# Kernel tuning notes

Hardware: AMD Instinct MI355X
Metric: run time of the kernel (lower is better)

Reference implementation:

```python
import jax, jax.numpy as jnp
import numpy as np

B, N, SNB, V = 1, 30000, 6, 4
IN_DIM, B_HID, B_OUT = 7, 256, 128
ENC_NODE, ENC_G = 128, 64
A_IN, A_HID = B_OUT + ENC_NODE + ENC_G, 256


def setup_inputs() -> dict:
    key = jax.random.key(0)
    ks = jax.random.split(key, 18)

    def w(k, shape, fan_in):
        return jax.random.normal(k, shape, dtype=jnp.float32) / np.sqrt(fan_in)

    return {
        "surface_mesh_centers": jax.random.normal(ks[0], (B, N, 3), dtype=jnp.float32),
        "encoding_g": jax.random.normal(ks[1], (B, N, ENC_G), dtype=jnp.float32),
        "encoding_node": jax.random.normal(ks[2], (B, N, ENC_NODE), dtype=jnp.float32),
        "surface_mesh_neighbors": jax.random.normal(ks[3], (B, N, SNB, 3), dtype=jnp.float32),
        "surface_normals": jax.random.normal(ks[4], (B, N, 3), dtype=jnp.float32),
        "surface_neighbors_normals": jax.random.normal(ks[5], (B, N, SNB, 3), dtype=jnp.float32),
        "surface_areas": jax.random.uniform(ks[6], (B, N, 1), dtype=jnp.float32, minval=0.1, maxval=1.0),
        "surface_neighbors_areas": jax.random.uniform(ks[7], (B, N, SNB, 1), dtype=jnp.float32, minval=0.1, maxval=1.0),
        "global_params_values": jax.random.normal(ks[8], (B, 2, 1), dtype=jnp.float32),
        "global_params_reference": jax.random.uniform(ks[9], (B, 2, 1), dtype=jnp.float32, minval=0.5, maxval=1.5),
        # per-variable nn_basis MLP params (stacked over V)
        "W1": w(ks[10], (V, IN_DIM, B_HID), IN_DIM),
        "b1": jnp.zeros((V, B_HID), dtype=jnp.float32),
        "W2": w(ks[11], (V, B_HID, B_OUT), B_HID),
        "b2": jnp.zeros((V, B_OUT), dtype=jnp.float32),
        # per-variable aggregation MLP params (stacked over V)
        "A1": w(ks[12], (V, A_IN, A_HID), A_IN),
        "Ab1": jnp.zeros((V, A_HID), dtype=jnp.float32),
        "A2": w(ks[13], (V, A_HID, 1), A_HID),
        "Ab2": jnp.zeros((V, 1), dtype=jnp.float32),
    }


def reference(surface_mesh_centers, encoding_g, encoding_node, surface_mesh_neighbors,
              surface_normals, surface_neighbors_normals, surface_areas,
              surface_neighbors_areas, global_params_values, global_params_reference,
              W1, b1, W2, b2, A1, Ab1, A2, Ab2):
    relu = jax.nn.relu
    # concat geometry features (use_surface_normals=True, use_surface_area=True)
    centers = jnp.concatenate(
        [surface_mesh_centers, surface_normals, jnp.log(surface_areas) / 10.0], axis=-1)  # [B,N,7]
    neighbors = jnp.concatenate(
        [surface_mesh_neighbors, surface_neighbors_normals,
         jnp.log(surface_neighbors_areas) / 10.0], axis=-1)  # [B,N,S,7]
    nb = neighbors + 1e-6  # surf_m_c for p>=1
    # inverse-distance weights (norm over full concatenated feature dim, as in source)
    dist = jnp.linalg.norm(centers[:, :, None, :] - nb, axis=-1, keepdims=True)  # [B,N,S,1]

    # nn_basis for all variables at once (ReLU hidden, linear out)
    basis_c = jnp.einsum('bni,vio->bvno', centers, W1) + b1[None, :, None, :]
    basis_c = jnp.einsum('bvno,voh->bvnh', relu(basis_c), W2) + b2[None, :, None, :]  # [B,V,N,BO]
    basis_nb = jnp.einsum('bnsi,vio->bvnso', nb, W1) + b1[None, :, None, None, :]
    basis_nb = jnp.einsum('bvnso,voh->bvnsh', relu(basis_nb), W2) + b2[None, :, None, None, :]  # [B,V,N,S,BO]

    # aggregation MLP; split first layer to avoid materializing concat(basis, enc_node, enc_g)
    A1b, A1n, A1g = A1[:, :B_OUT], A1[:, B_OUT:B_OUT + ENC_NODE], A1[:, B_OUT + ENC_NODE:]
    enc_pre = (jnp.einsum('bni,vih->bvnh', encoding_node, A1n)
               + jnp.einsum('bni,vih->bvnh', encoding_g, A1g)
               + Ab1[None, :, None, :])  # [B,V,N,H], shared across sample points
    h_c = relu(jnp.einsum('bvno,voh->bvnh', basis_c, A1b) + enc_pre)
    out_c = jnp.einsum('bvnh,vho->bvno', h_c, A2) + Ab2[None, :, None, :]  # [B,V,N,1]
    h_nb = relu(jnp.einsum('bvnso,voh->bvnsh', basis_nb, A1b) + enc_pre[:, :, :, None, :])
    out_nb = jnp.einsum('bvnsh,vho->bvnso', h_nb, A2) + Ab2[None, :, None, None, :]  # [B,V,N,S,1]

    inv = 1.0 / dist  # [B,N,S,1]
    out_neighbor = jnp.sum(out_nb * inv[:, None], axis=3)  # [B,V,N,1]
    dist_sum = jnp.sum(inv, axis=2)  # [B,N,1]
    out = 0.5 * out_c + 0.5 * out_neighbor / dist_sum[:, None]  # [B,V,N,1]
    return out[..., 0].transpose(0, 2, 1)  # [B,N,V]
```

## Files before the change

### kernel.cpp

```cpp
#include <hip/hip_runtime.h>
#include <hip/hip_bf16.h>
#include <math.h>

#define NT 16
#define RR 112
#define RP 128

typedef __attribute__((ext_vector_type(8))) short bf16x8;
typedef __attribute__((ext_vector_type(4))) float f32x4;

#define W1T_OFF 0
#define W1T_ELEMS (4*256*40)
#define W2T_OFF (W1T_OFF + W1T_ELEMS)
#define W2T_ELEMS (4*128*264)
#define A1T_OFF (W2T_OFF + W2T_ELEMS)
#define A1T_ELEMS (4*256*328)
#define WS_ELEMS (A1T_OFF + A1T_ELEMS)

__device__ __forceinline__ unsigned short f2b(float f) {
  union { float f; unsigned u; } x; x.f = f;
  unsigned r = x.u + 0x7fffu + ((x.u >> 16) & 1u);
  return (unsigned short)(r >> 16);
}
__device__ __forceinline__ float b2f(unsigned short h) {
  union { unsigned u; float f; } x; x.u = ((unsigned)h) << 16; return x.f;
}

__global__ void scs_prep(const float* __restrict__ W1, const float* __restrict__ W2,
                         const float* __restrict__ A1, unsigned short* __restrict__ ws) {
  for (int e = blockIdx.x * 256 + threadIdx.x; e < WS_ELEMS; e += gridDim.x * 256) {
    unsigned short val;
    if (e < W2T_OFF) {
      int r = e;            int v = r / (256*40); r %= (256*40);
      int o = r / 40, i = r % 40;
      val = (i < 7) ? f2b(W1[((size_t)v*7 + i)*256 + o]) : (unsigned short)0;
    } else if (e < A1T_OFF) {
      int r = e - W2T_OFF;  int v = r / (128*264); r %= (128*264);
      int h = r / 264, o = r % 264;
      val = (o < 256) ? f2b(W2[((size_t)v*256 + o)*128 + h]) : (unsigned short)0;
    } else {
      int r = e - A1T_OFF;  int v = r / (256*328); r %= (256*328);
      int h = r / 328, i = r % 328;
      val = (i < 320) ? f2b(A1[((size_t)v*320 + i)*256 + h]) : (unsigned short)0;
    }
    ws[e] = val;
  }
}

__global__ __launch_bounds__(256, 2)
void scs_fused(const float* __restrict__ centers_g,
               const float* __restrict__ enc_g,
               const float* __restrict__ enc_n,
               const float* __restrict__ nb_pos,
               const float* __restrict__ normals_g,
               const float* __restrict__ nb_norm,
               const float* __restrict__ areas_g,
               const float* __restrict__ nb_area,
               const unsigned short* __restrict__ ws,
               const float* __restrict__ b1,
               const float* __restrict__ b2,
               const float* __restrict__ Ab1,
               const float* __restrict__ A2,
               const float* __restrict__ Ab2,
               float* __restrict__ out,
               int Nn)
{
  const int v  = blockIdx.y;
  const int n0 = blockIdx.x * NT;
  const int t  = threadIdx.x;
  const int lane = t & 63;
  const int wv = t >> 6;
  const int lr = lane & 15;
  const int lk = lane >> 4;

  __shared__ unsigned short featb[RP * 40];
  __shared__ unsigned short h1s[RP * 72];
  __shared__ unsigned short basis[RP * 136];
  __shared__ unsigned short encA[NT * 200];
  __shared__ float inv_s[NT][8];
  __shared__ float rowpart[4][RP];

  for (int e = t; e < NT * 192; e += 256) {
    int row = e / 192, c = e % 192;
    int n = n0 + row; if (n >= Nn) n = Nn - 1;
    float val = (c < 128) ? enc_n[(size_t)n * 128 + c] : enc_g[(size_t)n * 64 + (c - 128)];
    encA[row * 200 + c] = f2b(val);
  }
  if (t < RP) {
    float f[8];
    #pragma unroll
    for (int i = 0; i < 8; i++) f[i] = 0.f;
    const int r = t;
    if (r < RR) {
      const int j = r / 7, p = r % 7;
      const int n = n0 + j;
      if (n < Nn) {
        if (p == 0) {
          f[0] = centers_g[(size_t)n*3+0]; f[1] = centers_g[(size_t)n*3+1]; f[2] = centers_g[(size_t)n*3+2];
          f[3] = normals_g[(size_t)n*3+0]; f[4] = normals_g[(size_t)n*3+1]; f[5] = normals_g[(size_t)n*3+2];
          f[6] = logf(areas_g[n]) * 0.1f;
        } else {
          const int s = p - 1;
          const float* mp = nb_pos  + ((size_t)n*6 + s)*3;
          const float* mn = nb_norm + ((size_t)n*6 + s)*3;
          f[0] = mp[0] + 1e-6f; f[1] = mp[1] + 1e-6f; f[2] = mp[2] + 1e-6f;
          f[3] = mn[0] + 1e-6f; f[4] = mn[1] + 1e-6f; f[5] = mn[2] + 1e-6f;
          f[6] = logf(nb_area[(size_t)n*6 + s]) * 0.1f + 1e-6f;
        }
      }
    }
    unsigned* fb32 = reinterpret_cast<unsigned*>(featb);
    #pragma unroll
    for (int i = 0; i < 4; i++) {
      unsigned lo = f2b(f[2*i]), hi = f2b(f[2*i+1]);
      fb32[r * 20 + i] = lo | (hi << 16);
    }
    #pragma unroll
    for (int i = 4; i < 20; i++) fb32[r * 20 + i] = 0;
  }
  __syncthreads();

  if (t < NT * 6) {
    const int j = t / 6, s = t % 6;
    float d2 = 0.f;
    #pragma unroll
    for (int i = 0; i < 7; i++) {
      const float d = b2f(featb[(j*7)*40 + i]) - b2f(featb[(j*7 + 1 + s)*40 + i]);
      d2 += d * d;
    }
    inv_s[j][s] = 1.f / sqrtf(d2);
  }

  f32x4 accB[8][2];
  {
    #pragma unroll
    for (int nt = 0; nt < 2; ++nt) {
      const float bb = b2[v*128 + wv*32 + nt*16 + lr];
      #pragma unroll
      for (int mt = 0; mt < 8; ++mt) accB[mt][nt] = (f32x4){bb, bb, bb, bb};
    }
  }
  const unsigned short* w1t = ws + W1T_OFF + (size_t)v * 256 * 40;
  const unsigned short* w2t = ws + W2T_OFF + (size_t)v * 128 * 264;

  for (int ch = 0; ch < 4; ++ch) {
    {
      const int obase = ch*64 + wv*16;
      const bf16x8 bfrag = *(const bf16x8*)(w1t + (size_t)(obase + lr)*40 + lk*8);
      const float b1c = b1[v*256 + obase + lr];
      #pragma unroll
      for (int mt = 0; mt < 8; ++mt) {
        const bf16x8 afrag = *(const bf16x8*)&featb[(mt*16 + lr)*40 + lk*8];
        f32x4 c = (f32x4){b1c, b1c, b1c, b1c};
        c = __builtin_amdgcn_mfma_f32_16x16x32_bf16(afrag, bfrag, c, 0, 0, 0);
        #pragma unroll
        for (int g = 0; g < 4; ++g)
          h1s[(mt*16 + lk*4 + g)*72 + wv*16 + lr] = f2b(fmaxf(c[g], 0.f));
      }
    }
    __syncthreads();
    #pragma unroll
    for (int ks = 0; ks < 2; ++ks) {
      bf16x8 bf[2];
      #pragma unroll
      for (int nt = 0; nt < 2; ++nt)
        bf[nt] = *(const bf16x8*)(w2t + (size_t)(wv*32 + nt*16 + lr)*264 + ch*64 + ks*32 + lk*8);
      #pragma unroll
      for (int mt = 0; mt < 8; ++mt) {
        const bf16x8 af = *(const bf16x8*)&h1s[(mt*16 + lr)*72 + ks*32 + lk*8];
        accB[mt][0] = __builtin_amdgcn_mfma_f32_16x16x32_bf16(af, bf[0], accB[mt][0], 0, 0, 0);
        accB[mt][1] = __builtin_amdgcn_mfma_f32_16x16x32_bf16(af, bf[1], accB[mt][1], 0, 0, 0);
      }
    }
    __syncthreads();
  }

  #pragma unroll
  for (int mt = 0; mt < 8; ++mt)
    #pragma unroll
    for (int nt = 0; nt < 2; ++nt)
      #pragma unroll
      for (int g = 0; g < 4; ++g)
        basis[(mt*16 + lk*4 + g)*136 + wv*32 + nt*16 + lr] = f2b(accB[mt][nt][g]);
  __syncthreads();

  f32x4 accH[8][4];
  const int nbase = wv * 64;
  {
    #pragma unroll
    for (int nt = 0; nt < 4; ++nt) {
      const float ab = Ab1[v*256 + nbase + nt*16 + lr];
      #pragma unroll
      for (int mt = 0; mt < 8; ++mt) accH[mt][nt] = (f32x4){ab, ab, ab, ab};
    }
  }
  int jrow[8];
  #pragma unroll
  for (int mt = 0; mt < 8; ++mt) {
    int row = mt*16 + lr;
    int j = row / 7; if (j > NT-1) j = NT-1;
    jrow[mt] = j;
  }
  const unsigned short* a1t = ws + A1T_OFF + (size_t)v * 256 * 328;
  #pragma unroll
  for (int ks = 0; ks < 4; ++ks) {
    bf16x8 bf[4];
    #pragma unroll
    for (int nt = 0; nt < 4; ++nt)
      bf[nt] = *(const bf16x8*)(a1t + (size_t)(nbase + nt*16 + lr)*328 + ks*32 + lk*8);
    #pragma unroll
    for (int mt = 0; mt < 8; ++mt) {
      const bf16x8 af = *(const bf16x8*)&basis[(mt*16 + lr)*136 + ks*32 + lk*8];
      #pragma unroll
      for (int nt = 0; nt < 4; ++nt)
        accH[mt][nt] = __builtin_amdgcn_mfma_f32_16x16x32_bf16(af, bf[nt], accH[mt][nt], 0, 0, 0);
    }
  }
  #pragma unroll
  for (int ks = 0; ks < 6; ++ks) {
    bf16x8 bf[4];
    #pragma unroll
    for (int nt = 0; nt < 4; ++nt)
      bf[nt] = *(const bf16x8*)(a1t + (size_t)(nbase + nt*16 + lr)*328 + (4 + ks)*32 + lk*8);
    #pragma unroll
    for (int mt = 0; mt < 8; ++mt) {
      const bf16x8 af = *(const bf16x8*)&encA[jrow[mt]*200 + ks*32 + lk*8];
      #pragma unroll
      for (int nt = 0; nt < 4; ++nt)
        accH[mt][nt] = __builtin_amdgcn_mfma_f32_16x16x32_bf16(af, bf[nt], accH[mt][nt], 0, 0, 0);
    }
  }

  {
    float a2c[4];
    #pragma unroll
    for (int nt = 0; nt < 4; ++nt) a2c[nt] = A2[v*256 + nbase + nt*16 + lr];
    #pragma unroll
    for (int mt = 0; mt < 8; ++mt) {
      #pragma unroll
      for (int g = 0; g < 4; ++g) {
        float s = 0.f;
        #pragma unroll
        for (int nt = 0; nt < 4; ++nt)
          s += fmaxf(accH[mt][nt][g], 0.f) * a2c[nt];
        s += __shfl_xor(s, 1); s += __shfl_xor(s, 2);
        s += __shfl_xor(s, 4); s += __shfl_xor(s, 8);
        if (lr == 0) rowpart[wv][mt*16 + lk*4 + g] = s;
      }
    }
  }
  __syncthreads();

  if (t < NT) {
    const int n = n0 + t;
    if (n < Nn) {
      const float ab2v = Ab2[v];
      float pt[7];
      #pragma unroll
      for (int p = 0; p < 7; ++p)
        pt[p] = rowpart[0][t*7+p] + rowpart[1][t*7+p] + rowpart[2][t*7+p] + rowpart[3][t*7+p] + ab2v;
      float snum = 0.f, sden = 0.f;
      #pragma unroll
      for (int s6 = 0; s6 < 6; ++s6) {
        const float iv = inv_s[t][s6];
        snum += pt[1 + s6] * iv; sden += iv;
      }
      out[(size_t)n*4 + v] = 0.5f * pt[0] + 0.5f * snum / sden;
    }
  }
}

extern "C" void kernel_launch(void* const* d_in, const int* in_sizes, int n_in,
                              void* d_out, int out_size, void* d_ws, size_t ws_size,
                              hipStream_t stream) {
  (void)n_in; (void)out_size; (void)ws_size;
  const float* centers = (const float*)d_in[0];
  const float* encg    = (const float*)d_in[1];
  const float* encn    = (const float*)d_in[2];
  const float* nbpos   = (const float*)d_in[3];
  const float* normals = (const float*)d_in[4];
  const float* nbnorm  = (const float*)d_in[5];
  const float* areas   = (const float*)d_in[6];
  const float* nbarea  = (const float*)d_in[7];
  const float* W1  = (const float*)d_in[10];
  const float* b1  = (const float*)d_in[11];
  const float* W2  = (const float*)d_in[12];
  const float* b2  = (const float*)d_in[13];
  const float* A1  = (const float*)d_in[14];
  const float* Ab1 = (const float*)d_in[15];
  const float* A2  = (const float*)d_in[16];
  const float* Ab2 = (const float*)d_in[17];
  float* out = (float*)d_out;
  unsigned short* ws = (unsigned short*)d_ws;

  const int Nn = in_sizes[0] / 3;

  hipLaunchKernelGGL(scs_prep, dim3(2000), dim3(256), 0, stream, W1, W2, A1, ws);

  dim3 grid((Nn + NT - 1) / NT, 4);
  hipLaunchKernelGGL(scs_fused, grid, dim3(256), 0, stream,
                     centers, encg, encn, nbpos, normals, nbnorm, areas, nbarea,
                     ws, b1, b2, Ab1, A2, Ab2, out, Nn);
}
```

Measured before the change: 454.2 us.

## Precompute per-node encoding projection once and shrink LDS for higher occupancy

The encoding-node/encoding-g part of the aggregation first layer is now computed once per node (16 rows) into an fp32 shared buffer and added in the epilogue. Before, it was recomputed for all 128 sample-point rows through MFMA, so this removes most of that MFMA work. The basis matrix is staged through the reused h1 buffer in two halves, the rowpart array aliases featb, and feature fragments are hoisted into registers. Launch bounds ask for 3 blocks per CU, which adds register pressure and a risk of spills. The prep grid size is also reduced.

Result: slower. 694.5 us (+52.9%).

```diff
diff --git a/kernel.cpp b/kernel.cpp
--- a/kernel.cpp
+++ b/kernel.cpp
@@ -47,7 +47,7 @@
   }
 }
 
-__global__ __launch_bounds__(256, 2)
+__global__ __launch_bounds__(256, 3)
 void scs_fused(const float* __restrict__ centers_g,
                const float* __restrict__ enc_g,
                const float* __restrict__ enc_n,
@@ -74,11 +74,11 @@
   const int lk = lane >> 4;
 
   __shared__ unsigned short featb[RP * 40];
-  __shared__ unsigned short h1s[RP * 72];
-  __shared__ unsigned short basis[RP * 136];
   __shared__ unsigned short encA[NT * 200];
+  __shared__ float encpre[NT * 260];
+  __shared__ unsigned short h1buf[RP * 72];
   __shared__ float inv_s[NT][8];
-  __shared__ float rowpart[4][RP];
+  float* rowpart = (float*)featb;
 
   for (int e = t; e < NT * 192; e += 256) {
     int row = e / 192, c = e % 192;
@@ -120,6 +120,11 @@
   }
   __syncthreads();
 
+  bf16x8 ffrag[8];
+  #pragma unroll
+  for (int mt = 0; mt < 8; ++mt)
+    ffrag[mt] = *(const bf16x8*)&featb[(mt*16 + lr)*40 + lk*8];
+
   if (t < NT * 6) {
     const int j = t / 6, s = t % 6;
     float d2 = 0.f;
@@ -131,17 +136,42 @@
     inv_s[j][s] = 1.f / sqrtf(d2);
   }
 
-  f32x4 accB[8][2];
+  const unsigned short* w1t = ws + W1T_OFF + (size_t)v * 256 * 40;
+  const unsigned short* w2t = ws + W2T_OFF + (size_t)v * 128 * 264;
+  const unsigned short* a1t = ws + A1T_OFF + (size_t)v * 256 * 328;
+
+  {
+    f32x4 acc_e[4];
+    #pragma unroll
+    for (int nt = 0; nt < 4; ++nt) {
+      const float ab = Ab1[v*256 + wv*64 + nt*16 + lr];
+      acc_e[nt] = (f32x4){ab, ab, ab, ab};
+    }
+    #pragma unroll
+    for (int ks = 0; ks < 6; ++ks) {
+      const bf16x8 af = *(const bf16x8*)&encA[lr*200 + ks*32 + lk*8];
+      #pragma unroll
+      for (int nt = 0; nt < 4; ++nt) {
+        const bf16x8 bf = *(const bf16x8*)(a1t + (size_t)(wv*64 + nt*16 + lr)*328 + 128 + ks*32 + lk*8);
+        acc_e[nt] = __builtin_amdgcn_mfma_f32_16x16x32_bf16(af, bf, acc_e[nt], 0, 0, 0);
+      }
+    }
+    #pragma unroll
+    for (int nt = 0; nt < 4; ++nt)
+      #pragma unroll
+      for (int g = 0; g < 4; ++g)
+        encpre[(lk*4 + g)*260 + wv*64 + nt*16 + lr] = acc_e[nt][g];
+  }
+
+  f32x4 acc_b[8][2];
   {
     #pragma unroll
     for (int nt = 0; nt < 2; ++nt) {
       const float bb = b2[v*128 + wv*32 + nt*16 + lr];
       #pragma unroll
-      for (int mt = 0; mt < 8; ++mt) accB[mt][nt] = (f32x4){bb, bb, bb, bb};
-    }
-  }
-  const unsigned short* w1t = ws + W1T_OFF + (size_t)v * 256 * 40;
-  const unsigned short* w2t = ws + W2T_OFF + (size_t)v * 128 * 264;
+      for (int mt = 0; mt < 8; ++mt) acc_b[mt][nt] = (f32x4){bb, bb, bb, bb};
+    }
+  }
 
   for (int ch = 0; ch < 4; ++ch) {
     {
@@ -150,102 +180,83 @@
       const float b1c = b1[v*256 + obase + lr];
       #pragma unroll
       for (int mt = 0; mt < 8; ++mt) {
-        const bf16x8 afrag = *(const bf16x8*)&featb[(mt*16 + lr)*40 + lk*8];
         f32x4 c = (f32x4){b1c, b1c, b1c, b1c};
-        c = __builtin_amdgcn_mfma_f32_16x16x32_bf16(afrag, bfrag, c, 0, 0, 0);
+        c = __builtin_amdgcn_mfma_f32_16x16x32_bf16(ffrag[mt], bfrag, c, 0, 0, 0);
         #pragma unroll
         for (int g = 0; g < 4; ++g)
-          h1s[(mt*16 + lk*4 + g)*72 + wv*16 + lr] = f2b(fmaxf(c[g], 0.f));
+          h1buf[(mt*16 + lk*4 + g)*72 + wv*16 + lr] = f2b(fmaxf(c[g], 0.f));
       }
     }
     __syncthreads();
     #pragma unroll
-    for (int ks = 0; ks < 2; ++ks) {
+    for (int ksl = 0; ksl < 2; ++ksl) {
       bf16x8 bf[2];
       #pragma unroll
       for (int nt = 0; nt < 2; ++nt)
-        bf[nt] = *(const bf16x8*)(w2t + (size_t)(wv*32 + nt*16 + lr)*264 + ch*64 + ks*32 + lk*8);
+        bf[nt] = *(const bf16x8*)(w2t + (size_t)(wv*32 + nt*16 + lr)*264 + ch*64 + ksl*32 + lk*8);
       #pragma unroll
       for (int mt = 0; mt < 8; ++mt) {
-        const bf16x8 af = *(const bf16x8*)&h1s[(mt*16 + lr)*72 + ks*32 + lk*8];
-        accB[mt][0] = __builtin_amdgcn_mfma_f32_16x16x32_bf16(af, bf[0], accB[mt][0], 0, 0, 0);
-        accB[mt][1] = __builtin_amdgcn_mfma_f32_16x16x32_bf16(af, bf[1], accB[mt][1], 0, 0, 0);
+        const bf16x8 af = *(const bf16x8*)&h1buf[(mt*16 + lr)*72 + ksl*32 + lk*8];
+        acc_b[mt][0] = __builtin_amdgcn_mfma_f32_16x16x32_bf16(af, bf[0], acc_b[mt][0], 0, 0, 0);
+        acc_b[mt][1] = __builtin_amdgcn_mfma_f32_16x16x32_bf16(af, bf[1], acc_b[mt][1], 0, 0, 0);
       }
     }
     __syncthreads();
   }
 
+  f32x4 acc_h[8][4];
   #pragma unroll
   for (int mt = 0; mt < 8; ++mt)
     #pragma unroll
-    for (int nt = 0; nt < 2; ++nt)
-      #pragma unroll
-      for (int g = 0; g < 4; ++g)
-        basis[(mt*16 + lk*4 + g)*136 + wv*32 + nt*16 + lr] = f2b(accB[mt][nt][g]);
-  __syncthreads();
-
-  f32x4 accH[8][4];
-  const int nbase = wv * 64;
-  {
-    #pragma unroll
-    for (int nt = 0; nt < 4; ++nt) {
-      const float ab = Ab1[v*256 + nbase + nt*16 + lr];
-      #pragma unroll
-      for (int mt = 0; mt < 8; ++mt) accH[mt][nt] = (f32x4){ab, ab, ab, ab};
-    }
-  }
-  int jrow[8];
+    for (int nt = 0; nt < 4; ++nt)
+      acc_h[mt][nt] = (f32x4){0.f, 0.f, 0.f, 0.f};
+
   #pragma unroll
-  for (int mt = 0; mt < 8; ++mt) {
-    int row = mt*16 + lr;
-    int j = row / 7; if (j > NT-1) j = NT-1;
-    jrow[mt] = j;
-  }
-  const unsigned short* a1t = ws + A1T_OFF + (size_t)v * 256 * 328;
-  #pragma unroll
-  for (int ks = 0; ks < 4; ++ks) {
-    bf16x8 bf[4];
-    #pragma unroll
-    for (int nt = 0; nt < 4; ++nt)
-      bf[nt] = *(const bf16x8*)(a1t + (size_t)(nbase + nt*16 + lr)*328 + ks*32 + lk*8);
-    #pragma unroll
-    for (int mt = 0; mt < 8; ++mt) {
-      const bf16x8 af = *(const bf16x8*)&basis[(mt*16 + lr)*136 + ks*32 + lk*8];
-      #pragma unroll
-      for (int nt = 0; nt < 4; ++nt)
-        accH[mt][nt] = __builtin_amdgcn_mfma_f32_16x16x32_bf16(af, bf[nt], accH[mt][nt], 0, 0, 0);
-    }
-  }
-  #pragma unroll
-  for (int ks = 0; ks < 6; ++ks) {
-    bf16x8 bf[4];
-    #pragma unroll
-    for (int nt = 0; nt < 4; ++nt)
-      bf[nt] = *(const bf16x8*)(a1t + (size_t)(nbase + nt*16 + lr)*328 + (4 + ks)*32 + lk*8);
-    #pragma unroll
-    for (int mt = 0; mt < 8; ++mt) {
-      const bf16x8 af = *(const bf16x8*)&encA[jrow[mt]*200 + ks*32 + lk*8];
-      #pragma unroll
-      for (int nt = 0; nt < 4; ++nt)
-        accH[mt][nt] = __builtin_amdgcn_mfma_f32_16x16x32_bf16(af, bf[nt], accH[mt][nt], 0, 0, 0);
-    }
+  for (int half = 0; half < 2; ++half) {
+    if ((wv >> 1) == half) {
+      #pragma unroll
+      for (int mt = 0; mt < 8; ++mt)
+        #pragma unroll
+        for (int nt = 0; nt < 2; ++nt)
+          #pragma unroll
+          for (int g = 0; g < 4; ++g)
+            h1buf[(mt*16 + lk*4 + g)*72 + (wv & 1)*32 + nt*16 + lr] = f2b(acc_b[mt][nt][g]);
+    }
+    __syncthreads();
+    #pragma unroll
+    for (int ksl = 0; ksl < 2; ++ksl) {
+      #pragma unroll
+      for (int nt = 0; nt < 4; ++nt) {
+        const bf16x8 bf = *(const bf16x8*)(a1t + (size_t)(wv*64 + nt*16 + lr)*328 + half*64 + ksl*32 + lk*8);
+        #pragma unroll
+        for (int mt = 0; mt < 8; ++mt) {
+          const bf16x8 af = *(const bf16x8*)&h1buf[(mt*16 + lr)*72 + ksl*32 + lk*8];
+          acc_h[mt][nt] = __builtin_amdgcn_mfma_f32_16x16x32_bf16(af, bf, acc_h[mt][nt], 0, 0, 0);
+        }
+      }
+    }
+    __syncthreads();
   }
 
   {
     float a2c[4];
     #pragma unroll
-    for (int nt = 0; nt < 4; ++nt) a2c[nt] = A2[v*256 + nbase + nt*16 + lr];
+    for (int nt = 0; nt < 4; ++nt) a2c[nt] = A2[v*256 + wv*64 + nt*16 + lr];
     #pragma unroll
     for (int mt = 0; mt < 8; ++mt) {
       #pragma unroll
       for (int g = 0; g < 4; ++g) {
+        const int row = mt*16 + lk*4 + g;
+        int j = row / 7; if (j > NT-1) j = NT-1;
         float s = 0.f;
         #pragma unroll
-        for (int nt = 0; nt < 4; ++nt)
-          s += fmaxf(accH[mt][nt][g], 0.f) * a2c[nt];
+        for (int nt = 0; nt < 4; ++nt) {
+          const float h2 = acc_h[mt][nt][g] + encpre[j*260 + wv*64 + nt*16 + lr];
+          s += fmaxf(h2, 0.f) * a2c[nt];
+        }
         s += __shfl_xor(s, 1); s += __shfl_xor(s, 2);
         s += __shfl_xor(s, 4); s += __shfl_xor(s, 8);
-        if (lr == 0) rowpart[wv][mt*16 + lk*4 + g] = s;
+        if (lr == 0) rowpart[wv*RP + row] = s;
       }
     }
   }
@@ -258,7 +269,8 @@
       float pt[7];
       #pragma unroll
       for (int p = 0; p < 7; ++p)
-        pt[p] = rowpart[0][t*7+p] + rowpart[1][t*7+p] + rowpart[2][t*7+p] + rowpart[3][t*7+p] + ab2v;
+        pt[p] = rowpart[0*RP + t*7+p] + rowpart[1*RP + t*7+p]
+              + rowpart[2*RP + t*7+p] + rowpart[3*RP + t*7+p] + ab2v;
       float snum = 0.f, sden = 0.f;
       #pragma unroll
       for (int s6 = 0; s6 < 6; ++s6) {
@@ -295,7 +307,7 @@
 
   const int Nn = in_sizes[0] / 3;
 
-  hipLaunchKernelGGL(scs_prep, dim3(2000), dim3(256), 0, stream, W1, W2, A1, ws);
+  hipLaunchKernelGGL(scs_prep, dim3(1024), dim3(256), 0, stream, W1, W2, A1, ws);
 
   dim3 grid((Nn + NT - 1) / NT, 4);
   hipLaunchKernelGGL(scs_fused, grid, dim3(256), 0, stream,
```
